# Optimization experiments

Hardware: AMD Instinct MI355X
Metric: run time of the kernel (lower is better)

## Reference

```python
import jax, jax.numpy as jnp
import numpy as np

B, S, I, H = 64, 512, 1024, 1024


def setup_inputs() -> dict:
    key = jax.random.key(0)
    ks = jax.random.split(key, 7)
    sc = 0.02
    return {
        "x": jax.random.normal(ks[0], (B, S, I), jnp.float32),
        "Wx0": jax.random.normal(ks[1], (I, 4 * H), jnp.float32) * sc,
        "Wh0": jax.random.normal(ks[2], (H, 4 * H), jnp.float32) * sc,
        "b0": jax.random.normal(ks[3], (4 * H,), jnp.float32) * sc,
        "Wx1": jax.random.normal(ks[4], (H, 4 * H), jnp.float32) * sc,
        "Wh1": jax.random.normal(ks[5], (H, 4 * H), jnp.float32) * sc,
        "b1": jax.random.normal(ks[6], (4 * H,), jnp.float32) * sc,
    }


def _lstm_layer(x_seq, Wx, Wh, b):
    """x_seq: (S, B, in). Gate order along 4H axis: i, f, g, o."""
    hid = Wh.shape[0]
    # Precompute input-side projections for all timesteps (one big GEMM).
    xg = jnp.einsum('sbi,ih->sbh', x_seq, Wx) + b  # (S, B, 4H)

    def step(carry, xg_t):
        h, c = carry
        g = xg_t + h @ Wh                      # (B, 4H)
        i, f, gg, o = jnp.split(g, 4, axis=-1)
        i = jax.nn.sigmoid(i)
        f = jax.nn.sigmoid(f)
        gg = jnp.tanh(gg)
        o = jax.nn.sigmoid(o)
        c = f * c + i * gg
        h = o * jnp.tanh(c)
        return (h, c), h

    bsz = x_seq.shape[1]
    h0 = jnp.zeros((bsz, hid), x_seq.dtype)
    c0 = jnp.zeros((bsz, hid), x_seq.dtype)
    (_, _), hs = jax.lax.scan(step, (h0, c0), xg)
    return hs  # (S, B, H)


def reference(x, Wx0, Wh0, b0, Wx1, Wh1, b1):
    # batch_first=True -> (B,S,I); internal layout is time-major (S,B,I)
    xs = jnp.swapaxes(x, 0, 1)
    h1 = _lstm_layer(xs, Wx0, Wh0, b0)
    h2 = _lstm_layer(h1, Wx1, Wh1, b1)
    return jnp.swapaxes(h2, 0, 1)  # (B, S, H)
```

## Files before the change

kernel.cpp:

```cpp
#include <hip/hip_runtime.h>
#include <hip/hip_bf16.h>

#define SEQ  512
#define HID  1024
#define G4   4096
#define NBLK 128

typedef short bf16x8 __attribute__((ext_vector_type(8)));
typedef float f32x4  __attribute__((ext_vector_type(4)));
typedef unsigned long long u64;

static __device__ __forceinline__ unsigned short f2b(float f) {
  union { float f; unsigned u; } v; v.f = f;
  unsigned r = (v.u + 0x7FFFu + ((v.u >> 16) & 1u)) >> 16;
  return (unsigned short)r;
}

__global__ __launch_bounds__(256) void k_castx(const float* __restrict__ x,
                                               unsigned short* __restrict__ xb) {
  int idx = blockIdx.x * 256 + threadIdx.x;
  int r = idx >> 8, kq = idx & 255;
  int b = r & 63, s = r >> 6;
  float4 v = *reinterpret_cast<const float4*>(x + ((size_t)b * SEQ + s) * HID + (size_t)kq * 4);
  ushort4 o;
  o.x = f2b(v.x); o.y = f2b(v.y); o.z = f2b(v.z); o.w = f2b(v.w);
  *reinterpret_cast<ushort4*>(xb + (size_t)r * HID + kq * 4) = o;
}

__global__ __launch_bounds__(256) void k_wtrans(const float* __restrict__ W,
                                                unsigned short* __restrict__ WT) {
  __shared__ float tls[32][33];
  int tile = blockIdx.x;
  int nt = tile & 127, kt = tile >> 7;
  int tx = threadIdx.x & 31, ty = threadIdx.x >> 5;
  int k0 = kt * 32, n0 = nt * 32;
  for (int i = 0; i < 4; ++i)
    tls[ty + 8 * i][tx] = W[(size_t)(k0 + ty + 8 * i) * G4 + n0 + tx];
  __syncthreads();
  for (int i = 0; i < 4; ++i)
    WT[(size_t)(n0 + ty + 8 * i) * HID + k0 + tx] = f2b(tls[tx][ty + 8 * i]);
}

static __device__ __forceinline__ void wave_wait8(unsigned* base, unsigned tgt) {
  unsigned* p = base + (threadIdx.x & 7) * 32;
  long sp = 0;
  for (;;) {
    unsigned v = __hip_atomic_load(p, __ATOMIC_RELAXED, __HIP_MEMORY_SCOPE_AGENT);
    if (__all(v >= tgt)) break;
    if (++sp > 10000000L) break;
    __builtin_amdgcn_s_sleep(1);
  }
  asm volatile("" ::: "memory");
}

static __device__ __forceinline__ void lds_wait(int* f, int tgt) {
  long sp = 0;
  while (__hip_atomic_load(f, __ATOMIC_RELAXED, __HIP_MEMORY_SCOPE_WORKGROUP) < tgt) {
    if (++sp > 200000000L) break;
    __builtin_amdgcn_s_sleep(1);
  }
  asm volatile("" ::: "memory");
}

__global__ __launch_bounds__(512, 1) void k_scan2(
    const unsigned short* __restrict__ xb,
    const unsigned short* __restrict__ WxT0, const unsigned short* __restrict__ WhT0,
    const float* __restrict__ b0,
    const unsigned short* __restrict__ WxT1, const unsigned short* __restrict__ WhT1,
    const float* __restrict__ b1,
    unsigned short* __restrict__ h1,
    unsigned short* __restrict__ h2, int h2mod,
    float* __restrict__ out,
    unsigned* __restrict__ bars) {
  __shared__ unsigned short wlds[32 * 2048];
  __shared__ float x_lds[2][4][8][64];
  __shared__ unsigned lds_arr;
  __shared__ int hrdy, xrdy;

  const int bk  = blockIdx.x;
  const int layer = bk >> 7;
  const int nb  = bk & 127;
  const int tid = threadIdx.x;
  const int w   = tid >> 6;
  const int l   = tid & 63;
  const int lq  = l >> 4, lr = l & 15;
  const int rt  = w & 3;
  const bool is_h = (w >= 4);

  const unsigned short* WxT = layer ? WxT1 : WxT0;
  const unsigned short* WhT = layer ? WhT1 : WhT0;
  const float* bias = layer ? b1 : b0;
  const unsigned short* aseq = layer ? h1 : xb;
  unsigned short* hout = layer ? h2 : h1;
  const int hmod = layer ? h2mod : 512;
  float* fout = layer ? out : nullptr;
  unsigned* ownbase = bars + layer * 256;
  unsigned* grpc = ownbase + (nb >> 4) * 32;

  if (tid == 0) { lds_arr = 0; hrdy = 0; xrdy = 0; }

  {
    int c = tid >> 4, seg = tid & 15;
    int gate = c >> 3, nl = c & 7;
    int gcol = gate * 1024 + nb * 8 + nl;
    const unsigned short* sx = WxT + (size_t)gcol * HID;
    const unsigned short* sh = WhT + (size_t)gcol * HID;
    for (int j = 0; j < 16; ++j) {
      int kk = seg * 128 + j * 8;
      const unsigned short* src = (kk < 1024) ? (sx + kk) : (sh + kk - 1024);
      uint4 v = *reinterpret_cast<const uint4*>(src);
      int db = (c * 4096 + kk * 2) ^ ((c & 7) << 4);
      *reinterpret_cast<uint4*>(reinterpret_cast<char*>(wlds) + db) = v;
    }
  }

  char* wbase = reinterpret_cast<char*>(wlds);
  const int csw = (lr & 7) << 4;
  const int cb0 = (lr) * 4096 + lq * 16;
  const int cb1 = (16 + lr) * 4096 + lq * 16;

  float bias_c[2];
#pragma unroll
  for (int ct = 0; ct < 2; ++ct) {
    int col = ct * 16 + lr;
    bias_c[ct] = bias[(col >> 3) * 1024 + nb * 8 + (col & 7)];
  }

  float cst[4] = {0.f, 0.f, 0.f, 0.f};

  __syncthreads();
  if (is_h) __builtin_amdgcn_s_setprio(1);

  if (!is_h) {
    if (layer) wave_wait8(bars, 16u);
    const bf16x8* ax = reinterpret_cast<const bf16x8*>(aseq) + (size_t)(rt * 16 + lr) * 128 + lq;
    f32x4 acc[2][4] = {};
#pragma unroll 8
    for (int ks = 0; ks < 32; ++ks) {
      bf16x8 a  = ax[ks * 4];
      bf16x8 bb0 = *reinterpret_cast<const bf16x8*>(wbase + ((cb0 + ks * 64) ^ csw));
      bf16x8 bb1 = *reinterpret_cast<const bf16x8*>(wbase + ((cb1 + ks * 64) ^ csw));
      acc[0][ks & 3] = __builtin_amdgcn_mfma_f32_16x16x32_bf16(a, bb0, acc[0][ks & 3], 0, 0, 0);
      acc[1][ks & 3] = __builtin_amdgcn_mfma_f32_16x16x32_bf16(a, bb1, acc[1][ks & 3], 0, 0, 0);
    }
#pragma unroll
    for (int ct = 0; ct < 2; ++ct) {
      f32x4 s = (acc[ct][0] + acc[ct][1]) + (acc[ct][2] + acc[ct][3]);
      float bc = bias_c[ct];
      x_lds[0][w][ct * 4 + 0][l] = s.x + bc;
      x_lds[0][w][ct * 4 + 1][l] = s.y + bc;
      x_lds[0][w][ct * 4 + 2][l] = s.z + bc;
      x_lds[0][w][ct * 4 + 3][l] = s.w + bc;
    }
  }
  __syncthreads();

  for (int t = 0; t < SEQ; ++t) {
    if (!is_h) {
      if (t + 1 < SEQ) {
        if (layer) {
          if (w == 0) {
            wave_wait8(bars, 16u * (unsigned)(t + 2));
            __hip_atomic_store(&xrdy, t + 1, __ATOMIC_RELAXED, __HIP_MEMORY_SCOPE_WORKGROUP);
          } else {
            lds_wait(&xrdy, t + 1);
          }
        }
        const bf16x8* ax = reinterpret_cast<const bf16x8*>(aseq)
                           + ((size_t)(t + 1) * 64 + rt * 16 + lr) * 128 + lq;
        f32x4 acc[2][4] = {};
#pragma unroll 8
        for (int ks = 0; ks < 32; ++ks) {
          bf16x8 a  = ax[ks * 4];
          bf16x8 bb0 = *reinterpret_cast<const bf16x8*>(wbase + ((cb0 + ks * 64) ^ csw));
          bf16x8 bb1 = *reinterpret_cast<const bf16x8*>(wbase + ((cb1 + ks * 64) ^ csw));
          acc[0][ks & 3] = __builtin_amdgcn_mfma_f32_16x16x32_bf16(a, bb0, acc[0][ks & 3], 0, 0, 0);
          acc[1][ks & 3] = __builtin_amdgcn_mfma_f32_16x16x32_bf16(a, bb1, acc[1][ks & 3], 0, 0, 0);
        }
        int bn2 = (t + 1) & 1;
#pragma unroll
        for (int ct = 0; ct < 2; ++ct) {
          f32x4 s = (acc[ct][0] + acc[ct][1]) + (acc[ct][2] + acc[ct][3]);
          float bc = bias_c[ct];
          x_lds[bn2][w][ct * 4 + 0][l] = s.x + bc;
          x_lds[bn2][w][ct * 4 + 1][l] = s.y + bc;
          x_lds[bn2][w][ct * 4 + 2][l] = s.z + bc;
          x_lds[bn2][w][ct * 4 + 3][l] = s.w + bc;
        }
      }
    } else {
      const int bn = t & 1;
      f32x4 acc[2][4];
#pragma unroll
      for (int ct = 0; ct < 2; ++ct) {
        acc[ct][0] = f32x4{x_lds[bn][rt][ct * 4 + 0][l], x_lds[bn][rt][ct * 4 + 1][l],
                           x_lds[bn][rt][ct * 4 + 2][l], x_lds[bn][rt][ct * 4 + 3][l]};
        acc[ct][1] = f32x4{0.f, 0.f, 0.f, 0.f};
        acc[ct][2] = f32x4{0.f, 0.f, 0.f, 0.f};
        acc[ct][3] = f32x4{0.f, 0.f, 0.f, 0.f};
      }

      if (t > 0) {
        if (w == 4) {
          wave_wait8(ownbase, 16u * (unsigned)t);
          __hip_atomic_store(&hrdy, t, __ATOMIC_RELAXED, __HIP_MEMORY_SCOPE_WORKGROUP);
        } else {
          lds_wait(&hrdy, t);
        }
        const size_t hbase = (size_t)((t - 1) % hmod) * (64 * HID) + (size_t)(rt * 16 + lr) * HID;
        if (hmod != 4) {
          const bf16x8* hp = reinterpret_cast<const bf16x8*>(hout + hbase) + lq;
#pragma unroll 8
          for (int ks = 0; ks < 32; ++ks) {
            bf16x8 a = hp[ks * 4];
            bf16x8 bb0 = *reinterpret_cast<const bf16x8*>(wbase + ((cb0 + 2048 + ks * 64) ^ csw));
            bf16x8 bb1 = *reinterpret_cast<const bf16x8*>(wbase + ((cb1 + 2048 + ks * 64) ^ csw));
            acc[0][ks & 3] = __builtin_amdgcn_mfma_f32_16x16x32_bf16(a, bb0, acc[0][ks & 3], 0, 0, 0);
            acc[1][ks & 3] = __builtin_amdgcn_mfma_f32_16x16x32_bf16(a, bb1, acc[1][ks & 3], 0, 0, 0);
          }
        } else {
          const u64* hp = reinterpret_cast<const u64*>(hout + hbase) + lq * 2;
#pragma unroll 8
          for (int ks = 0; ks < 32; ++ks) {
            u64 q0 = __hip_atomic_load(hp + ks * 8,     __ATOMIC_RELAXED, __HIP_MEMORY_SCOPE_AGENT);
            u64 q1 = __hip_atomic_load(hp + ks * 8 + 1, __ATOMIC_RELAXED, __HIP_MEMORY_SCOPE_AGENT);
            union { u64 q[2]; bf16x8 v; } u; u.q[0] = q0; u.q[1] = q1;
            bf16x8 bb0 = *reinterpret_cast<const bf16x8*>(wbase + ((cb0 + 2048 + ks * 64) ^ csw));
            bf16x8 bb1 = *reinterpret_cast<const bf16x8*>(wbase + ((cb1 + 2048 + ks * 64) ^ csw));
            acc[0][ks & 3] = __builtin_amdgcn_mfma_f32_16x16x32_bf16(u.v, bb0, acc[0][ks & 3], 0, 0, 0);
            acc[1][ks & 3] = __builtin_amdgcn_mfma_f32_16x16x32_bf16(u.v, bb1, acc[1][ks & 3], 0, 0, 0);
          }
        }
      }

      f32x4 s0 = (acc[0][0] + acc[0][1]) + (acc[0][2] + acc[0][3]);
      f32x4 s1 = (acc[1][0] + acc[1][1]) + (acc[1][2] + acc[1][3]);
      float a0[4] = {s0.x, s0.y, s0.z, s0.w};
      float a1[4] = {s1.x, s1.y, s1.z, s1.w};
      float b0r[4], b1r[4];
#pragma unroll
      for (int r = 0; r < 4; ++r) {
        b0r[r] = __shfl_xor(a0[r], 8, 64);
        b1r[r] = __shfl_xor(a1[r], 8, 64);
      }
      const bool isX = ((l & 8) == 0);
      float hvf[4];
#pragma unroll
      for (int r = 0; r < 4; ++r) {
        float gi = isX ? a0[r] : b0r[r];
        float gf = isX ? b0r[r] : a0[r];
        float gg = isX ? a1[r] : b1r[r];
        float go = isX ? b1r[r] : a1[r];
        float ig = 1.f / (1.f + __expf(-gi));
        float fg = 1.f / (1.f + __expf(-gf));
        float e2 = __expf(2.f * gg);
        float gv = (e2 - 1.f) / (e2 + 1.f);
        float og = 1.f / (1.f + __expf(-go));
        cst[r] = fg * cst[r] + ig * gv;
        float e2c = __expf(2.f * cst[r]);
        hvf[r] = og * (e2c - 1.f) / (e2c + 1.f);
      }
      float hn[4];
#pragma unroll
      for (int r = 0; r < 4; ++r) hn[r] = __shfl_xor(hvf[r], 1, 64);
      const bool ev = ((l & 1) == 0);
      unsigned pk[4]; float he[4], ho[4];
#pragma unroll
      for (int r = 0; r < 4; ++r) {
        he[r] = ev ? hvf[r] : hn[r];
        ho[r] = ev ? hn[r] : hvf[r];
        pk[r] = (unsigned)f2b(he[r]) | ((unsigned)f2b(ho[r]) << 16);
      }
      const int sub = ((l >> 3) & 1) * 2 + (l & 1);
      unsigned pks = sub == 0 ? pk[0] : sub == 1 ? pk[1] : sub == 2 ? pk[2] : pk[3];
      const int row = rt * 16 + lq * 4 + sub;
      const int cp  = (lr & 7) >> 1;
      unsigned* hw = reinterpret_cast<unsigned*>(hout + (size_t)(t % hmod) * (64 * HID))
                     + (size_t)row * 512 + nb * 4 + cp;
      __hip_atomic_store(hw, pks, __ATOMIC_RELAXED, __HIP_MEMORY_SCOPE_AGENT);
      if (fout) {
        float hes = sub == 0 ? he[0] : sub == 1 ? he[1] : sub == 2 ? he[2] : he[3];
        float hos = sub == 0 ? ho[0] : sub == 1 ? ho[1] : sub == 2 ? ho[2] : ho[3];
        *reinterpret_cast<float2*>(fout + (size_t)row * (SEQ * HID) + (size_t)t * HID
                                   + nb * 8 + cp * 2) = make_float2(hes, hos);
      }

      asm volatile("s_waitcnt vmcnt(0)" ::: "memory");
      if (l == 0) {
        unsigned pb = atomicAdd(&lds_arr, 1u);
        if ((pb & 3) == 3)
          __hip_atomic_fetch_add(grpc, 1u, __ATOMIC_RELAXED, __HIP_MEMORY_SCOPE_AGENT);
      }
    }
    __syncthreads();
  }
}

extern "C" void kernel_launch(void* const* d_in, const int* in_sizes, int n_in,
                              void* d_out, int out_size, void* d_ws, size_t ws_size,
                              hipStream_t stream) {
  const float* x   = (const float*)d_in[0];
  const float* Wx0 = (const float*)d_in[1];
  const float* Wh0 = (const float*)d_in[2];
  const float* b0  = (const float*)d_in[3];
  const float* Wx1 = (const float*)d_in[4];
  const float* Wh1 = (const float*)d_in[5];
  const float* b1  = (const float*)d_in[6];
  float* out = (float*)d_out;
  char* ws = (char*)d_ws;

  unsigned short* xb   = (unsigned short*)(ws);
  unsigned short* h1   = (unsigned short*)(ws + 67108864);
  unsigned short* WxT0 = (unsigned short*)(ws + 134217728);
  unsigned short* WhT0 = (unsigned short*)(ws + 142606336);
  unsigned short* WxT1 = (unsigned short*)(ws + 150994944);
  unsigned short* WhT1 = (unsigned short*)(ws + 159383552);
  unsigned* bars       = (unsigned*)(ws + 167772160);
  unsigned short* h2   = (unsigned short*)(ws + 167776256);
  int h2mod = (ws_size >= (size_t)167776256 + 67108864) ? 512 : 4;

  hipMemsetAsync(bars, 0, 4096, stream);
  k_castx<<<32768, 256, 0, stream>>>(x, xb);
  k_wtrans<<<4096, 256, 0, stream>>>(Wx0, WxT0);
  k_wtrans<<<4096, 256, 0, stream>>>(Wh0, WhT0);
  k_wtrans<<<4096, 256, 0, stream>>>(Wx1, WxT1);
  k_wtrans<<<4096, 256, 0, stream>>>(Wh1, WhT1);
  k_scan2<<<2 * NBLK, 512, 0, stream>>>(xb, WxT0, WhT0, b0, WxT1, WhT1, b1,
                                        h1, h2, h2mod, out, bars);
}
```

Measured before the change: 5.081 ms.

## Replace grouped atomic-add barrier counters with per-block step flags polled by one wave

Each block now publishes its completed timestep by storing to its own padded flag, where before it did an atomic fetch-add on a counter shared by 16 blocks. Waiters poll all 128 flags of a layer with two loads per lane, instead of 8 group counters. The flag is published right after the h stores and before the fp32 output write, which takes that write off the critical path. This is meant to remove atomic contention on shared counters and shorten inter-block step latency, in exchange for more polling traffic and a serial wait inside wave 4 for the other waves' arrival.

```diff
diff --git a/kernel.cpp b/kernel.cpp
--- a/kernel.cpp
+++ b/kernel.cpp
@@ -41,13 +41,16 @@
     WT[(size_t)(n0 + ty + 8 * i) * HID + k0 + tx] = f2b(tls[tx][ty + 8 * i]);
 }
 
-static __device__ __forceinline__ void wave_wait8(unsigned* base, unsigned tgt) {
-  unsigned* p = base + (threadIdx.x & 7) * 32;
+static __device__ __forceinline__ void poll_flags128(unsigned* flags, unsigned tgt) {
+  const int l = threadIdx.x & 63;
+  unsigned* p0 = flags + l * 32;
+  unsigned* p1 = flags + (64 + l) * 32;
   long sp = 0;
   for (;;) {
-    unsigned v = __hip_atomic_load(p, __ATOMIC_RELAXED, __HIP_MEMORY_SCOPE_AGENT);
-    if (__all(v >= tgt)) break;
-    if (++sp > 10000000L) break;
+    unsigned v0 = __hip_atomic_load(p0, __ATOMIC_RELAXED, __HIP_MEMORY_SCOPE_AGENT);
+    unsigned v1 = __hip_atomic_load(p1, __ATOMIC_RELAXED, __HIP_MEMORY_SCOPE_AGENT);
+    if (__all((v0 >= tgt) && (v1 >= tgt))) break;
+    if (++sp > 2000000L) break;
     __builtin_amdgcn_s_sleep(1);
   }
   asm volatile("" ::: "memory");
@@ -56,7 +59,7 @@
 static __device__ __forceinline__ void lds_wait(int* f, int tgt) {
   long sp = 0;
   while (__hip_atomic_load(f, __ATOMIC_RELAXED, __HIP_MEMORY_SCOPE_WORKGROUP) < tgt) {
-    if (++sp > 200000000L) break;
+    if (++sp > 50000000L) break;
     __builtin_amdgcn_s_sleep(1);
   }
   asm volatile("" ::: "memory");
@@ -94,8 +97,9 @@
   unsigned short* hout = layer ? h2 : h1;
   const int hmod = layer ? h2mod : 512;
   float* fout = layer ? out : nullptr;
-  unsigned* ownbase = bars + layer * 256;
-  unsigned* grpc = ownbase + (nb >> 4) * 32;
+  unsigned* ownflags = bars + layer * 4096;
+  unsigned* l0flags  = bars;
+  unsigned* myflag   = ownflags + nb * 32;
 
   if (tid == 0) { lds_arr = 0; hrdy = 0; xrdy = 0; }
 
@@ -132,7 +136,7 @@
   if (is_h) __builtin_amdgcn_s_setprio(1);
 
   if (!is_h) {
-    if (layer) wave_wait8(bars, 16u);
+    if (layer) poll_flags128(l0flags, 1u);
     const bf16x8* ax = reinterpret_cast<const bf16x8*>(aseq) + (size_t)(rt * 16 + lr) * 128 + lq;
     f32x4 acc[2][4] = {};
 #pragma unroll 8
@@ -160,7 +164,7 @@
       if (t + 1 < SEQ) {
         if (layer) {
           if (w == 0) {
-            wave_wait8(bars, 16u * (unsigned)(t + 2));
+            poll_flags128(l0flags, (unsigned)(t + 2));
             __hip_atomic_store(&xrdy, t + 1, __ATOMIC_RELAXED, __HIP_MEMORY_SCOPE_WORKGROUP);
           } else {
             lds_wait(&xrdy, t + 1);
@@ -202,7 +206,7 @@
 
       if (t > 0) {
         if (w == 4) {
-          wave_wait8(ownbase, 16u * (unsigned)t);
+          poll_flags128(ownflags, (unsigned)t);
           __hip_atomic_store(&hrdy, t, __ATOMIC_RELAXED, __HIP_MEMORY_SCOPE_WORKGROUP);
         } else {
           lds_wait(&hrdy, t);
@@ -278,18 +282,26 @@
       unsigned* hw = reinterpret_cast<unsigned*>(hout + (size_t)(t % hmod) * (64 * HID))
                      + (size_t)row * 512 + nb * 4 + cp;
       __hip_atomic_store(hw, pks, __ATOMIC_RELAXED, __HIP_MEMORY_SCOPE_AGENT);
+
+      asm volatile("s_waitcnt vmcnt(0)" ::: "memory");
+      if (l == 0) {
+        atomicAdd(&lds_arr, 1u);
+        if (w == 4) {
+          long sp = 0;
+          while (__hip_atomic_load(&lds_arr, __ATOMIC_RELAXED, __HIP_MEMORY_SCOPE_WORKGROUP)
+                 < 4u * (unsigned)(t + 1)) {
+            if (++sp > 50000000L) break;
+            __builtin_amdgcn_s_sleep(1);
+          }
+          __hip_atomic_store(myflag, (unsigned)(t + 1), __ATOMIC_RELAXED, __HIP_MEMORY_SCOPE_AGENT);
+        }
+      }
+
       if (fout) {
         float hes = sub == 0 ? he[0] : sub == 1 ? he[1] : sub == 2 ? he[2] : he[3];
         float hos = sub == 0 ? ho[0] : sub == 1 ? ho[1] : sub == 2 ? ho[2] : ho[3];
         *reinterpret_cast<float2*>(fout + (size_t)row * (SEQ * HID) + (size_t)t * HID
                                    + nb * 8 + cp * 2) = make_float2(hes, hos);
-      }
-
-      asm volatile("s_waitcnt vmcnt(0)" ::: "memory");
-      if (l == 0) {
-        unsigned pb = atomicAdd(&lds_arr, 1u);
-        if ((pb & 3) == 3)
-          __hip_atomic_fetch_add(grpc, 1u, __ATOMIC_RELAXED, __HIP_MEMORY_SCOPE_AGENT);
       }
     }
     __syncthreads();
@@ -316,10 +328,10 @@
   unsigned short* WxT1 = (unsigned short*)(ws + 150994944);
   unsigned short* WhT1 = (unsigned short*)(ws + 159383552);
   unsigned* bars       = (unsigned*)(ws + 167772160);
-  unsigned short* h2   = (unsigned short*)(ws + 167776256);
-  int h2mod = (ws_size >= (size_t)167776256 + 67108864) ? 512 : 4;
-
-  hipMemsetAsync(bars, 0, 4096, stream);
+  unsigned short* h2   = (unsigned short*)(ws + 167804928);
+  int h2mod = (ws_size >= (size_t)167804928 + 67108864) ? 512 : 4;
+
+  hipMemsetAsync(bars, 0, 32768, stream);
   k_castx<<<32768, 256, 0, stream>>>(x, xb);
   k_wtrans<<<4096, 256, 0, stream>>>(Wx0, WxT0);
   k_wtrans<<<4096, 256, 0, stream>>>(Wh0, WhT0);
```

New measurement: 4.788 ms. 1.06x faster.

## Replace grouped barrier counters with per-block step flags and chunked polling

Applied to the files above, without the earlier changes.

Swaps the two-level counter barrier (an LDS arrival counter feeding one global counter per group of 16 blocks) for per-block monotonic step flags. Each wave polls only the 32 producer flags covering the K-chunk it is about to consume, so MFMA work on early chunks can start before every producer has finished. The LDS broadcast flags and the sleep in the spin loops are removed. The fp32 output write moves off the recurrent h-waves onto the x-waves, which reread the bf16 h one step later. That last change also means the output is now rounded to bf16, and polling without sleep adds memory traffic.

```diff
diff --git a/kernel.cpp b/kernel.cpp
--- a/kernel.cpp
+++ b/kernel.cpp
@@ -14,6 +14,12 @@
   union { float f; unsigned u; } v; v.f = f;
   unsigned r = (v.u + 0x7FFFu + ((v.u >> 16) & 1u)) >> 16;
   return (unsigned short)r;
+}
+static __device__ __forceinline__ float b2f_lo(unsigned u) {
+  union { unsigned u; float f; } v; v.u = u << 16; return v.f;
+}
+static __device__ __forceinline__ float b2f_hi(unsigned u) {
+  union { unsigned u; float f; } v; v.u = u & 0xFFFF0000u; return v.f;
 }
 
 __global__ __launch_bounds__(256) void k_castx(const float* __restrict__ x,
@@ -41,23 +47,13 @@
     WT[(size_t)(n0 + ty + 8 * i) * HID + k0 + tx] = f2b(tls[tx][ty + 8 * i]);
 }
 
-static __device__ __forceinline__ void wave_wait8(unsigned* base, unsigned tgt) {
-  unsigned* p = base + (threadIdx.x & 7) * 32;
+static __device__ __forceinline__ void poll32(unsigned* row, unsigned tgt) {
+  unsigned* p = row + (threadIdx.x & 31);
   long sp = 0;
   for (;;) {
     unsigned v = __hip_atomic_load(p, __ATOMIC_RELAXED, __HIP_MEMORY_SCOPE_AGENT);
     if (__all(v >= tgt)) break;
-    if (++sp > 10000000L) break;
-    __builtin_amdgcn_s_sleep(1);
-  }
-  asm volatile("" ::: "memory");
-}
-
-static __device__ __forceinline__ void lds_wait(int* f, int tgt) {
-  long sp = 0;
-  while (__hip_atomic_load(f, __ATOMIC_RELAXED, __HIP_MEMORY_SCOPE_WORKGROUP) < tgt) {
-    if (++sp > 200000000L) break;
-    __builtin_amdgcn_s_sleep(1);
+    if (++sp > 3000000L) break;
   }
   asm volatile("" ::: "memory");
 }
@@ -74,8 +70,6 @@
     unsigned* __restrict__ bars) {
   __shared__ unsigned short wlds[32 * 2048];
   __shared__ float x_lds[2][4][8][64];
-  __shared__ unsigned lds_arr;
-  __shared__ int hrdy, xrdy;
 
   const int bk  = blockIdx.x;
   const int layer = bk >> 7;
@@ -94,10 +88,9 @@
   unsigned short* hout = layer ? h2 : h1;
   const int hmod = layer ? h2mod : 512;
   float* fout = layer ? out : nullptr;
-  unsigned* ownbase = bars + layer * 256;
-  unsigned* grpc = ownbase + (nb >> 4) * 32;
-
-  if (tid == 0) { lds_arr = 0; hrdy = 0; xrdy = 0; }
+  unsigned* frow_l0 = bars + rt * 128;
+  unsigned* frow_own = bars + (layer * 4 + rt) * 128;
+  unsigned* myflag = frow_own + nb;
 
   {
     int c = tid >> 4, seg = tid & 15;
@@ -132,16 +125,19 @@
   if (is_h) __builtin_amdgcn_s_setprio(1);
 
   if (!is_h) {
-    if (layer) wave_wait8(bars, 16u);
     const bf16x8* ax = reinterpret_cast<const bf16x8*>(aseq) + (size_t)(rt * 16 + lr) * 128 + lq;
     f32x4 acc[2][4] = {};
-#pragma unroll 8
-    for (int ks = 0; ks < 32; ++ks) {
-      bf16x8 a  = ax[ks * 4];
-      bf16x8 bb0 = *reinterpret_cast<const bf16x8*>(wbase + ((cb0 + ks * 64) ^ csw));
-      bf16x8 bb1 = *reinterpret_cast<const bf16x8*>(wbase + ((cb1 + ks * 64) ^ csw));
-      acc[0][ks & 3] = __builtin_amdgcn_mfma_f32_16x16x32_bf16(a, bb0, acc[0][ks & 3], 0, 0, 0);
-      acc[1][ks & 3] = __builtin_amdgcn_mfma_f32_16x16x32_bf16(a, bb1, acc[1][ks & 3], 0, 0, 0);
+#pragma unroll
+    for (int c = 0; c < 4; ++c) {
+      if (layer) poll32(frow_l0 + c * 32, 1u);
+#pragma unroll
+      for (int ks = c * 8; ks < c * 8 + 8; ++ks) {
+        bf16x8 a  = ax[ks * 4];
+        bf16x8 bb0 = *reinterpret_cast<const bf16x8*>(wbase + ((cb0 + ks * 64) ^ csw));
+        bf16x8 bb1 = *reinterpret_cast<const bf16x8*>(wbase + ((cb1 + ks * 64) ^ csw));
+        acc[0][ks & 3] = __builtin_amdgcn_mfma_f32_16x16x32_bf16(a, bb0, acc[0][ks & 3], 0, 0, 0);
+        acc[1][ks & 3] = __builtin_amdgcn_mfma_f32_16x16x32_bf16(a, bb1, acc[1][ks & 3], 0, 0, 0);
+      }
     }
 #pragma unroll
     for (int ct = 0; ct < 2; ++ct) {
@@ -158,24 +154,20 @@
   for (int t = 0; t < SEQ; ++t) {
     if (!is_h) {
       if (t + 1 < SEQ) {
-        if (layer) {
-          if (w == 0) {
-            wave_wait8(bars, 16u * (unsigned)(t + 2));
-            __hip_atomic_store(&xrdy, t + 1, __ATOMIC_RELAXED, __HIP_MEMORY_SCOPE_WORKGROUP);
-          } else {
-            lds_wait(&xrdy, t + 1);
-          }
-        }
         const bf16x8* ax = reinterpret_cast<const bf16x8*>(aseq)
                            + ((size_t)(t + 1) * 64 + rt * 16 + lr) * 128 + lq;
         f32x4 acc[2][4] = {};
-#pragma unroll 8
-        for (int ks = 0; ks < 32; ++ks) {
-          bf16x8 a  = ax[ks * 4];
-          bf16x8 bb0 = *reinterpret_cast<const bf16x8*>(wbase + ((cb0 + ks * 64) ^ csw));
-          bf16x8 bb1 = *reinterpret_cast<const bf16x8*>(wbase + ((cb1 + ks * 64) ^ csw));
-          acc[0][ks & 3] = __builtin_amdgcn_mfma_f32_16x16x32_bf16(a, bb0, acc[0][ks & 3], 0, 0, 0);
-          acc[1][ks & 3] = __builtin_amdgcn_mfma_f32_16x16x32_bf16(a, bb1, acc[1][ks & 3], 0, 0, 0);
+#pragma unroll
+        for (int c = 0; c < 4; ++c) {
+          if (layer) poll32(frow_l0 + c * 32, (unsigned)(t + 2));
+#pragma unroll
+          for (int ks = c * 8; ks < c * 8 + 8; ++ks) {
+            bf16x8 a  = ax[ks * 4];
+            bf16x8 bb0 = *reinterpret_cast<const bf16x8*>(wbase + ((cb0 + ks * 64) ^ csw));
+            bf16x8 bb1 = *reinterpret_cast<const bf16x8*>(wbase + ((cb1 + ks * 64) ^ csw));
+            acc[0][ks & 3] = __builtin_amdgcn_mfma_f32_16x16x32_bf16(a, bb0, acc[0][ks & 3], 0, 0, 0);
+            acc[1][ks & 3] = __builtin_amdgcn_mfma_f32_16x16x32_bf16(a, bb1, acc[1][ks & 3], 0, 0, 0);
+          }
         }
         int bn2 = (t + 1) & 1;
 #pragma unroll
@@ -188,6 +180,16 @@
           x_lds[bn2][w][ct * 4 + 3][l] = s.w + bc;
         }
       }
+      if (fout && t > 0) {
+        int tc = t - 1;
+        const unsigned* sp32 = reinterpret_cast<const unsigned*>(
+            hout + (size_t)(tc % hmod) * (64 * HID)) + (size_t)l * 512 + nb * 4 + rt;
+        unsigned pv = (hmod == 4)
+            ? __hip_atomic_load(sp32, __ATOMIC_RELAXED, __HIP_MEMORY_SCOPE_AGENT)
+            : *sp32;
+        *reinterpret_cast<float2*>(fout + (size_t)l * (SEQ * HID) + (size_t)tc * HID
+                                   + nb * 8 + rt * 2) = make_float2(b2f_lo(pv), b2f_hi(pv));
+      }
     } else {
       const int bn = t & 1;
       f32x4 acc[2][4];
@@ -201,34 +203,36 @@
       }
 
       if (t > 0) {
-        if (w == 4) {
-          wave_wait8(ownbase, 16u * (unsigned)t);
-          __hip_atomic_store(&hrdy, t, __ATOMIC_RELAXED, __HIP_MEMORY_SCOPE_WORKGROUP);
-        } else {
-          lds_wait(&hrdy, t);
-        }
         const size_t hbase = (size_t)((t - 1) % hmod) * (64 * HID) + (size_t)(rt * 16 + lr) * HID;
         if (hmod != 4) {
           const bf16x8* hp = reinterpret_cast<const bf16x8*>(hout + hbase) + lq;
-#pragma unroll 8
-          for (int ks = 0; ks < 32; ++ks) {
-            bf16x8 a = hp[ks * 4];
-            bf16x8 bb0 = *reinterpret_cast<const bf16x8*>(wbase + ((cb0 + 2048 + ks * 64) ^ csw));
-            bf16x8 bb1 = *reinterpret_cast<const bf16x8*>(wbase + ((cb1 + 2048 + ks * 64) ^ csw));
-            acc[0][ks & 3] = __builtin_amdgcn_mfma_f32_16x16x32_bf16(a, bb0, acc[0][ks & 3], 0, 0, 0);
-            acc[1][ks & 3] = __builtin_amdgcn_mfma_f32_16x16x32_bf16(a, bb1, acc[1][ks & 3], 0, 0, 0);
+#pragma unroll
+          for (int c = 0; c < 4; ++c) {
+            poll32(frow_own + c * 32, (unsigned)t);
+#pragma unroll
+            for (int ks = c * 8; ks < c * 8 + 8; ++ks) {
+              bf16x8 a = hp[ks * 4];
+              bf16x8 bb0 = *reinterpret_cast<const bf16x8*>(wbase + ((cb0 + 2048 + ks * 64) ^ csw));
+              bf16x8 bb1 = *reinterpret_cast<const bf16x8*>(wbase + ((cb1 + 2048 + ks * 64) ^ csw));
+              acc[0][ks & 3] = __builtin_amdgcn_mfma_f32_16x16x32_bf16(a, bb0, acc[0][ks & 3], 0, 0, 0);
+              acc[1][ks & 3] = __builtin_amdgcn_mfma_f32_16x16x32_bf16(a, bb1, acc[1][ks & 3], 0, 0, 0);
+            }
           }
         } else {
           const u64* hp = reinterpret_cast<const u64*>(hout + hbase) + lq * 2;
-#pragma unroll 8
-          for (int ks = 0; ks < 32; ++ks) {
-            u64 q0 = __hip_atomic_load(hp + ks * 8,     __ATOMIC_RELAXED, __HIP_MEMORY_SCOPE_AGENT);
-            u64 q1 = __hip_atomic_load(hp + ks * 8 + 1, __ATOMIC_RELAXED, __HIP_MEMORY_SCOPE_AGENT);
-            union { u64 q[2]; bf16x8 v; } u; u.q[0] = q0; u.q[1] = q1;
-            bf16x8 bb0 = *reinterpret_cast<const bf16x8*>(wbase + ((cb0 + 2048 + ks * 64) ^ csw));
-            bf16x8 bb1 = *reinterpret_cast<const bf16x8*>(wbase + ((cb1 + 2048 + ks * 64) ^ csw));
-            acc[0][ks & 3] = __builtin_amdgcn_mfma_f32_16x16x32_bf16(u.v, bb0, acc[0][ks & 3], 0, 0, 0);
-            acc[1][ks & 3] = __builtin_amdgcn_mfma_f32_16x16x32_bf16(u.v, bb1, acc[1][ks & 3], 0, 0, 0);
+#pragma unroll
+          for (int c = 0; c < 4; ++c) {
+            poll32(frow_own + c * 32, (unsigned)t);
+#pragma unroll
+            for (int ks = c * 8; ks < c * 8 + 8; ++ks) {
+              u64 q0 = __hip_atomic_load(hp + ks * 8,     __ATOMIC_RELAXED, __HIP_MEMORY_SCOPE_AGENT);
+              u64 q1 = __hip_atomic_load(hp + ks * 8 + 1, __ATOMIC_RELAXED, __HIP_MEMORY_SCOPE_AGENT);
+              union { u64 q[2]; bf16x8 v; } u; u.q[0] = q0; u.q[1] = q1;
+              bf16x8 bb0 = *reinterpret_cast<const bf16x8*>(wbase + ((cb0 + 2048 + ks * 64) ^ csw));
+              bf16x8 bb1 = *reinterpret_cast<const bf16x8*>(wbase + ((cb1 + 2048 + ks * 64) ^ csw));
+              acc[0][ks & 3] = __builtin_amdgcn_mfma_f32_16x16x32_bf16(u.v, bb0, acc[0][ks & 3], 0, 0, 0);
+              acc[1][ks & 3] = __builtin_amdgcn_mfma_f32_16x16x32_bf16(u.v, bb1, acc[1][ks & 3], 0, 0, 0);
+            }
           }
         }
       }
@@ -264,12 +268,12 @@
 #pragma unroll
       for (int r = 0; r < 4; ++r) hn[r] = __shfl_xor(hvf[r], 1, 64);
       const bool ev = ((l & 1) == 0);
-      unsigned pk[4]; float he[4], ho[4];
+      unsigned pk[4];
 #pragma unroll
       for (int r = 0; r < 4; ++r) {
-        he[r] = ev ? hvf[r] : hn[r];
-        ho[r] = ev ? hn[r] : hvf[r];
-        pk[r] = (unsigned)f2b(he[r]) | ((unsigned)f2b(ho[r]) << 16);
+        float he = ev ? hvf[r] : hn[r];
+        float ho = ev ? hn[r] : hvf[r];
+        pk[r] = (unsigned)f2b(he) | ((unsigned)f2b(ho) << 16);
       }
       const int sub = ((l >> 3) & 1) * 2 + (l & 1);
       unsigned pks = sub == 0 ? pk[0] : sub == 1 ? pk[1] : sub == 2 ? pk[2] : pk[3];
@@ -278,21 +282,22 @@
       unsigned* hw = reinterpret_cast<unsigned*>(hout + (size_t)(t % hmod) * (64 * HID))
                      + (size_t)row * 512 + nb * 4 + cp;
       __hip_atomic_store(hw, pks, __ATOMIC_RELAXED, __HIP_MEMORY_SCOPE_AGENT);
-      if (fout) {
-        float hes = sub == 0 ? he[0] : sub == 1 ? he[1] : sub == 2 ? he[2] : he[3];
-        float hos = sub == 0 ? ho[0] : sub == 1 ? ho[1] : sub == 2 ? ho[2] : ho[3];
-        *reinterpret_cast<float2*>(fout + (size_t)row * (SEQ * HID) + (size_t)t * HID
-                                   + nb * 8 + cp * 2) = make_float2(hes, hos);
-      }
 
       asm volatile("s_waitcnt vmcnt(0)" ::: "memory");
-      if (l == 0) {
-        unsigned pb = atomicAdd(&lds_arr, 1u);
-        if ((pb & 3) == 3)
-          __hip_atomic_fetch_add(grpc, 1u, __ATOMIC_RELAXED, __HIP_MEMORY_SCOPE_AGENT);
-      }
+      if (l == 0)
+        __hip_atomic_store(myflag, (unsigned)(t + 1), __ATOMIC_RELAXED, __HIP_MEMORY_SCOPE_AGENT);
     }
     __syncthreads();
+  }
+
+  if (!is_h && fout) {
+    const unsigned* sp32 = reinterpret_cast<const unsigned*>(
+        hout + (size_t)(511 % hmod) * (64 * HID)) + (size_t)l * 512 + nb * 4 + rt;
+    unsigned pv = (hmod == 4)
+        ? __hip_atomic_load(sp32, __ATOMIC_RELAXED, __HIP_MEMORY_SCOPE_AGENT)
+        : *sp32;
+    *reinterpret_cast<float2*>(fout + (size_t)l * (SEQ * HID) + (size_t)511 * HID
+                               + nb * 8 + rt * 2) = make_float2(b2f_lo(pv), b2f_hi(pv));
   }
 }
 
@@ -316,10 +321,10 @@
   unsigned short* WxT1 = (unsigned short*)(ws + 150994944);
   unsigned short* WhT1 = (unsigned short*)(ws + 159383552);
   unsigned* bars       = (unsigned*)(ws + 167772160);
-  unsigned short* h2   = (unsigned short*)(ws + 167776256);
-  int h2mod = (ws_size >= (size_t)167776256 + 67108864) ? 512 : 4;
-
-  hipMemsetAsync(bars, 0, 4096, stream);
+  unsigned short* h2   = (unsigned short*)(ws + 167804928);
+  int h2mod = (ws_size >= (size_t)167804928 + 67108864) ? 512 : 4;
+
+  hipMemsetAsync(bars, 0, 32768, stream);
   k_castx<<<32768, 256, 0, stream>>>(x, xb);
   k_wtrans<<<4096, 256, 0, stream>>>(Wx0, WxT0);
   k_wtrans<<<4096, 256, 0, stream>>>(Wh0, WhT0);
```

Measured after the change: 5.574 ms. 1.1x slower.
